# Performance work log

Measured on AMD Instinct MI355X. Metric: run time of the kernel, lower is better.

## Reference

```python
import jax, jax.numpy as jnp
import numpy as np

NC = 4
X = Y = Z = 64
IMG_SHAPE = (96, 96, 96)
SPAN = 2          # FILTER_SIZE = [5,5,5]
NUM_ITER = 4
DIL = 2           # DILATION = 2.0
SMOOTH_DISTANCE_INIT = 0.3
PRIOR_DISTANCE_INIT = 0.3


def _ind(d):
    # mirrors _get_ind from the torch code
    return (d, 0) if d > 0 else (0, -d)


def _sl(a, b):
    # slice(a, -b) with -0 -> None, mirrors _negative
    return slice(a, -b if b else None)


def _offsets():
    for dx in range(-SPAN, SPAN + 1):
        for dy in range(-SPAN, SPAN + 1):
            for dz in range(-SPAN, SPAN + 1):
                yield dx, dy, dz


def _lin_resize_axis(x, axis, out):
    # 1D linear interpolation matching torch align_corners=True
    n = x.shape[axis]
    if out == n:
        return x
    pos = jnp.arange(out, dtype=x.dtype) * ((n - 1) / (out - 1))
    i0 = jnp.clip(jnp.floor(pos).astype(jnp.int32), 0, n - 1)
    i1 = jnp.clip(i0 + 1, 0, n - 1)
    w = pos - i0.astype(x.dtype)
    shp = [1] * x.ndim
    shp[axis] = out
    w = w.reshape(shp)
    return jnp.take(x, i0, axis=axis) * (1 - w) + jnp.take(x, i1, axis=axis) * w


def _resize3d(x, out_sz):
    # trilinear, align_corners=True, separable over the 3 spatial axes of [b,c,X,Y,Z]
    for ax, o in zip((2, 3, 4), out_sz):
        x = _lin_resize_axis(x, ax, o)
    return x


def _smooth_gaussian(feats):
    # feats: [b, c, X, Y, Z] -> gaussian [b, 5,5,5, X, Y, Z]
    b = feats.shape[0]
    sp = feats.shape[2:]
    g = jnp.zeros((b, 5, 5, 5) + sp, feats.dtype)
    for dx, dy, dz in _offsets():
        dx1, dx2 = _ind(dx); dy1, dy2 = _ind(dy); dz1, dz2 = _ind(dz)
        a = feats[:, :, _sl(dx1, dx2), _sl(dy1, dy2), _sl(dz1, dz2)]
        c = feats[:, :, _sl(dx2, dx1), _sl(dy2, dy1), _sl(dz2, dz1)]
        e = jnp.exp(-0.5 * jnp.sum((a - c) ** 2, axis=1))
        g = g.at[:, dx + SPAN, dy + SPAN, dz + SPAN,
                 _sl(dx2, dx1), _sl(dy2, dy1), _sl(dz2, dz1)].set(e)
    return g


def _prior_gaussian(f1, f2):
    # f1, f2: [b, c, x, y, z] (already downsampled) -> [b, 5,5,5, x, y, z]
    b = f1.shape[0]
    sp = f1.shape[2:]
    g = jnp.zeros((b, 5, 5, 5) + sp, f1.dtype)
    for dx, dy, dz in _offsets():
        dx1, dx2 = _ind(dx); dy1, dy2 = _ind(dy); dz1, dz2 = _ind(dz)
        a = f1[:, :, _sl(dx2, dx1), _sl(dy2, dy1), _sl(dz2, dz1)]
        c = f2[:, :, _sl(dx1, dx2), _sl(dy1, dy2), _sl(dz1, dz2)]
        e = jnp.exp(-0.5 * jnp.sum((a - c) ** 2, axis=1))
        g = g.at[:, dx + SPAN, dy + SPAN, dz + SPAN,
                 _sl(dx2, dx1), _sl(dy2, dy1), _sl(dz2, dz1)].set(e)
    return g


def _message(p, g):
    # p: [b, nc, x, y, z]; g: [b, 5,5,5, x, y, z]
    out = jnp.zeros_like(p)
    for dx, dy, dz in _offsets():
        dx1, dx2 = _ind(dx); dy1, dy2 = _ind(dy); dz1, dz2 = _ind(dz)
        a = p[:, :, _sl(dx1, dx2), _sl(dy1, dy2), _sl(dz1, dz2)]
        w = g[:, None, dx + SPAN, dy + SPAN, dz + SPAN,
              _sl(dx2, dx1), _sl(dy2, dy1), _sl(dz2, dz1)]
        out = out.at[:, :, _sl(dx2, dx1), _sl(dy2, dy1), _sl(dz2, dz1)].add(a * w)
    return out


def setup_inputs() -> dict:
    key = jax.random.key(0)
    ks = jax.random.split(key, 6)
    unary = jax.random.normal(ks[0], (1, NC, X, Y, Z), jnp.float32)
    img = jax.random.normal(ks[1], (1, 2, X, Y, Z), jnp.float32)
    atlas = jax.random.normal(ks[2], (1, 2, X, Y, Z), jnp.float32)
    atlas_label = jax.random.uniform(ks[3], (1, X, Y, Z, NC), jnp.float32)
    patch_start = jax.random.randint(ks[4], (1, 3), 0, 32, jnp.int32)
    return {
        "unary": unary,
        "img": img,
        "atlas": atlas,
        "atlas_label": atlas_label,
        "patch_start": patch_start,
        "smooth_norm": jnp.array([1.0 / SMOOTH_DISTANCE_INIT], jnp.float32),
        "smooth_weight": jnp.ones((NC,), jnp.float32),
        "prior_norm": jnp.array([1.0 / PRIOR_DISTANCE_INIT], jnp.float32),
        "prior_weight": jnp.ones(IMG_SHAPE, jnp.float32),
        "compat_w": jnp.eye(NC, dtype=jnp.float32),
    }


def reference(unary, img, atlas, atlas_label, patch_start,
              smooth_norm, smooth_weight, prior_norm, prior_weight, compat_w):
    b, nc, x, y, z = unary.shape
    ds = (x // DIL, y // DIL, z // DIL)  # floor(in*0.5) == ceil(in/2) for even dims

    # similarity kernels
    sg = _smooth_gaussian(img * smooth_norm)                      # [b,5,5,5,x,y,z]
    f1 = _resize3d(img * prior_norm, ds)
    f2 = _resize3d(atlas * prior_norm, ds)
    pg = _prior_gaussian(f1, f2)                                  # [b,5,5,5,x/2,y/2,z/2]

    # prior message is independent of q_values: compute once
    al = jnp.transpose(atlas_label, (0, 4, 1, 2, 3))              # [b,nc,x,y,z]
    al_ds = _resize3d(al, ds)
    pm = _resize3d(_message(al_ds, pg), (x, y, z))                # [b,nc,x,y,z]
    pw = jax.lax.dynamic_slice(
        prior_weight,
        (patch_start[0, 0], patch_start[0, 1], patch_start[0, 2]),
        (x, y, z))
    prior_term = pw[None, None] * pm

    q = unary
    for _ in range(NUM_ITER):
        p = jax.nn.softmax(q, axis=1)
        sm = _message(p, sg)
        pred = smooth_weight[None, :, None, None, None] * sm + prior_term
        q = unary + jnp.einsum('oc,bcxyz->boxyz', compat_w, pred)  # 1x1x1 compat conv
    return q
```

## Files before the change

kernel.cpp:

```cpp
#include <hip/hip_runtime.h>

#define NN 64
#define N3 (64*64*64)
#define DS 32
#define DS3 (32*32*32)

#define LOG2E 1.4426950408889634f
#define FSCALE 0.8493218002880191f

typedef _Float16 h2  __attribute__((ext_vector_type(2)));
typedef __fp16   h2f __attribute__((ext_vector_type(2)));

__device__ __forceinline__ float fexp2(float x) { return __builtin_amdgcn_exp2f(x); }

__device__ __forceinline__ h2 u2h(unsigned u) { union { unsigned u; h2 h; } c; c.u = u; return c.h; }
__device__ __forceinline__ unsigned h2u(h2 h) { union { unsigned u; h2 h; } c; c.h = h; return c.u; }
__device__ __forceinline__ h2 pkh(float a, float b) {
    union { h2f a; h2 b; } c; c.a = __builtin_amdgcn_cvt_pkrtz(a, b); return c.b;
}
__device__ __forceinline__ float fdot2(h2 a, h2 b) {
    union { h2 h; h2f f; } ca, cb; ca.h = a; cb.h = b;
    return __builtin_amdgcn_fdot2(ca.f, cb.f, 0.0f, false);
}

__device__ __forceinline__ void axw(int j, float scale, int nmax, int& i0, int& i1, float& w) {
    float pos = (float)j * scale;
    int f = (int)floorf(pos);
    if (f < 0) f = 0;
    if (f > nmax) f = nmax;
    i0 = f;
    i1 = (f + 1 <= nmax) ? f + 1 : nmax;
    w = pos - (float)f;
}


__global__ __launch_bounds__(128) void k_downsample(
    const float* __restrict__ img, const float* __restrict__ atlas,
    const float* __restrict__ alabel, const float* __restrict__ pnorm,
    unsigned* __restrict__ f1pk, uint4* __restrict__ nb)
{
    int idx = blockIdx.x * 128 + threadIdx.x;
    int z = idx & 31, y = (idx >> 5) & 31, x = idx >> 10;

    const float scale = 63.0f / 31.0f;
    int x0,x1,y0,y1,z0,z1; float wx,wy,wz;
    axw(x, scale, 63, x0, x1, wx);
    axw(y, scale, 63, y0, y1, wy);
    axw(z, scale, 63, z0, z1, wz);

    float w000=(1-wx)*(1-wy)*(1-wz), w001=(1-wx)*(1-wy)*wz;
    float w010=(1-wx)*wy*(1-wz),     w011=(1-wx)*wy*wz;
    float w100=wx*(1-wy)*(1-wz),     w101=wx*(1-wy)*wz;
    float w110=wx*wy*(1-wz),         w111=wx*wy*wz;

    int c000=(x0*NN+y0)*NN+z0, c001=(x0*NN+y0)*NN+z1;
    int c010=(x0*NN+y1)*NN+z0, c011=(x0*NN+y1)*NN+z1;
    int c100=(x1*NN+y0)*NN+z0, c101=(x1*NN+y0)*NN+z1;
    int c110=(x1*NN+y1)*NN+z0, c111=(x1*NN+y1)*NN+z1;

    auto tri = [&](const float* p) -> float {
        return p[c000]*w000 + p[c001]*w001 + p[c010]*w010 + p[c011]*w011
             + p[c100]*w100 + p[c101]*w101 + p[c110]*w110 + p[c111]*w111;
    };
    float pnf = pnorm[0] * FSCALE;
    f1pk[idx] = h2u(pkh(pnf*tri(img), pnf*tri(img + N3)));

    auto tril = [&](int c) -> float {
        return alabel[c000*4+c]*w000 + alabel[c001*4+c]*w001 + alabel[c010*4+c]*w010 + alabel[c011*4+c]*w011
             + alabel[c100*4+c]*w100 + alabel[c101*4+c]*w101 + alabel[c110*4+c]*w110 + alabel[c111*4+c]*w111;
    };
    nb[idx] = make_uint4(h2u(pkh(pnf*tri(atlas), pnf*tri(atlas + N3))),
                         h2u(pkh(tril(0), tril(1))),
                         h2u(pkh(tril(2), tril(3))), 0u);
}

__global__ __launch_bounds__(128) void k_prior_msg(
    const unsigned* __restrict__ f1pk, const uint4* __restrict__ nb,
    float4* __restrict__ pm)
{
    int idx = blockIdx.x * 128 + threadIdx.x;
    int z = idx & 31, y = (idx >> 5) & 31, x = idx >> 10;

    h2 ncf = -u2h(f1pk[idx]);
    float a0=0.f, a1=0.f, a2=0.f, a3=0.f;
    for (int dx = -2; dx <= 2; ++dx) {
        int xx = x + dx; if ((unsigned)xx >= DS) continue;
        for (int dy = -2; dy <= 2; ++dy) {
            int yy = y + dy; if ((unsigned)yy >= DS) continue;
            int base = (xx*DS + yy)*DS;
            #pragma unroll
            for (int dz = -2; dz <= 2; ++dz) {
                int zz = z + dz; if ((unsigned)zz >= DS) continue;
                uint4 v = nb[base + zz];
                h2 d = u2h(v.x) + ncf;
                float t = fdot2(d, d);
                float w = fexp2(-t);
                h2 l01 = u2h(v.y), l23 = u2h(v.z);
                a0 += w*(float)l01.x; a1 += w*(float)l01.y;
                a2 += w*(float)l23.x; a3 += w*(float)l23.y;
            }
        }
    }
    pm[idx] = make_float4(a0, a1, a2, a3);
}


#define TXD 8
#define TYD 8
#define TZD 8
#define TZR 4
#define RZ 2
#define HX 12
#define HY 12
#define HZ 12
#define PZ 14

template<bool QV_IN, bool QV_OUT>
__global__ __launch_bounds__(1024, 8) void k_iter(
    const float* __restrict__ qin,
    const float* __restrict__ unary,
    const float* __restrict__ img,
    const float* __restrict__ snorm,
    const float* __restrict__ sweight,
    const float* __restrict__ compat,
    const float4* __restrict__ pm,
    const float* __restrict__ pweight,
    const int* __restrict__ pstart,
    float* __restrict__ qout)
{
    __shared__ __align__(16) uint2    pS[HX][HY][PZ];
    __shared__ __align__(8)  unsigned fS[HX][HY][PZ];
    __shared__ __align__(16) uint4    accS[3][TXD*TYD*TZR];

    const int tzg = threadIdx.x, ty = threadIdx.y;
    const int tx = threadIdx.z & 7, s = threadIdx.z >> 3;
    const int x0b = blockIdx.z * TXD, y0b = blockIdx.y * TYD, z0b = blockIdx.x * TZD;
    const int tid = threadIdx.x + TZR*threadIdx.y + (TZR*TYD)*threadIdx.z;
    const float sc = snorm[0] * FSCALE;

    #pragma unroll
    for (int rr = 0; rr < 2; ++rr) {
        int i = tid + rr*1024;
        if (i < HX*HY*HZ) {
            int lz = i % HZ; int r = i / HZ;
            int ly = r % HY; int lx = r / HY;
            int gx = x0b + lx - 2, gy = y0b + ly - 2, gz = z0b + lz - 2;
            uint2 pu = make_uint2(0u, 0u);
            unsigned fu = 0u;
            if ((unsigned)gx < NN && (unsigned)gy < NN && (unsigned)gz < NN) {
                int g = (gx*NN + gy)*NN + gz;
                float q0, q1, q2, q3;
                if (QV_IN) {
                    float4 qv = reinterpret_cast<const float4*>(qin)[g];
                    q0 = qv.x; q1 = qv.y; q2 = qv.z; q3 = qv.w;
                } else {
                    q0 = qin[g]; q1 = qin[g+N3]; q2 = qin[g+2*N3]; q3 = qin[g+3*N3];
                }
                float m = fmaxf(fmaxf(q0,q1), fmaxf(q2,q3));
                float e0 = fexp2((q0-m)*LOG2E);
                float e1 = fexp2((q1-m)*LOG2E);
                float e2 = fexp2((q2-m)*LOG2E);
                float e3 = fexp2((q3-m)*LOG2E);
                float inv = 1.0f/(e0+e1+e2+e3);
                pu = make_uint2(h2u(pkh(e0*inv, e1*inv)), h2u(pkh(e2*inv, e3*inv)));
                fu = h2u(pkh(img[g]*sc, img[g+N3]*sc));
            }
            pS[lx][ly][lz] = pu;
            fS[lx][ly][lz] = fu;
        }
    }
    __syncthreads();

    const int tz0 = tzg * RZ;
    const int gx = x0b + tx, gy = y0b + ty, gz = z0b + tz0;

    const h2 ncf0 = -u2h(fS[tx+2][ty+2][tz0+2]);
    const h2 ncf1 = -u2h(fS[tx+2][ty+2][tz0+3]);

    h2 a01_0 = (h2)0, a23_0 = (h2)0, a01_1 = (h2)0, a23_1 = (h2)0;

    #pragma unroll
    for (int pp = 0; pp < 7; ++pp) {
        int p = (3 - s) + 4*pp;
        if (p < 25) {
            int dx = p / 5, dy = p - 5*dx;
            const uint4* pv = reinterpret_cast<const uint4*>(&pS[tx+dx][ty+dy][tz0]);
            const uint2* fv = reinterpret_cast<const uint2*>(&fS[tx+dx][ty+dy][tz0]);
            uint4 qa = pv[0], qb = pv[1], qc = pv[2];
            uint2 fa = fv[0], fb = fv[1], fc = fv[2];

            unsigned fz[6]  = { fa.x, fa.y, fb.x, fb.y, fc.x, fc.y };
            unsigned p01[6] = { qa.x, qa.z, qb.x, qb.z, qc.x, qc.z };
            unsigned p23[6] = { qa.y, qa.w, qb.y, qb.w, qc.y, qc.w };

            #pragma unroll
            for (int dz = 0; dz < 5; ++dz) {
                {
                    h2 d = u2h(fz[dz]) + ncf0;
                    float w = fexp2(-fdot2(d, d));
                    h2 w2 = pkh(w, w);
                    a01_0 = w2 * u2h(p01[dz]) + a01_0;
                    a23_0 = w2 * u2h(p23[dz]) + a23_0;
                }
                {
                    h2 d = u2h(fz[dz+1]) + ncf1;
                    float w = fexp2(-fdot2(d, d));
                    h2 w2 = pkh(w, w);
                    a01_1 = w2 * u2h(p01[dz+1]) + a01_1;
                    a23_1 = w2 * u2h(p23[dz+1]) + a23_1;
                }
            }
        }
    }

    const int pid = (tx*TYD + ty)*TZR + tzg;
    if (s != 0) {
        accS[s-1][pid] = make_uint4(h2u(a01_0), h2u(a23_0), h2u(a01_1), h2u(a23_1));
    }

    float4 pr0 = make_float4(0.f,0.f,0.f,0.f), pr1 = make_float4(0.f,0.f,0.f,0.f);
    if (s == 0) {
        const float S13 = 31.0f / 63.0f;
        float posx = (float)gx * S13; int xc0 = (int)posx; float wxf = posx - (float)xc0;
        int xc1 = xc0 < 31 ? xc0+1 : 31;
        float posy = (float)gy * S13; int yc0 = (int)posy; float wyf = posy - (float)yc0;
        int yc1 = yc0 < 31 ? yc0+1 : 31;
        int r00i = (xc0*DS+yc0)*DS, r01i = (xc0*DS+yc1)*DS;
        int r10i = (xc1*DS+yc0)*DS, r11i = (xc1*DS+yc1)*DS;
        auto upz = [&](int gzv) -> float4 {
            float posz = (float)gzv * S13; int zc0 = (int)posz; float wzf = posz - (float)zc0;
            int zc1 = zc0 < 31 ? zc0+1 : 31;
            float4 p000 = pm[r00i+zc0], p001 = pm[r00i+zc1];
            float4 p010 = pm[r01i+zc0], p011 = pm[r01i+zc1];
            float4 p100 = pm[r10i+zc0], p101 = pm[r10i+zc1];
            float4 p110 = pm[r11i+zc0], p111 = pm[r11i+zc1];
            float w000=(1-wxf)*(1-wyf)*(1-wzf), w001=(1-wxf)*(1-wyf)*wzf;
            float w010=(1-wxf)*wyf*(1-wzf),     w011=(1-wxf)*wyf*wzf;
            float w100=wxf*(1-wyf)*(1-wzf),     w101=wxf*(1-wyf)*wzf;
            float w110=wxf*wyf*(1-wzf),         w111=wxf*wyf*wzf;
            float4 r;
            r.x = w000*p000.x + w001*p001.x + w010*p010.x + w011*p011.x + w100*p100.x + w101*p101.x + w110*p110.x + w111*p111.x;
            r.y = w000*p000.y + w001*p001.y + w010*p010.y + w011*p011.y + w100*p100.y + w101*p101.y + w110*p110.y + w111*p111.y;
            r.z = w000*p000.z + w001*p001.z + w010*p010.z + w011*p011.z + w100*p100.z + w101*p101.z + w110*p110.z + w111*p111.z;
            r.w = w000*p000.w + w001*p001.w + w010*p010.w + w011*p011.w + w100*p100.w + w101*p101.w + w110*p110.w + w111*p111.w;
            return r;
        };
        pr0 = upz(gz);
        pr1 = upz(gz+1);
        int ps0 = pstart[0], ps1 = pstart[1], ps2 = pstart[2];
        int pwbase = (ps0+gx)*96*96 + (ps1+gy)*96 + ps2 + gz;
        float pwa = pweight[pwbase], pwb = pweight[pwbase+1];
        pr0.x *= pwa; pr0.y *= pwa; pr0.z *= pwa; pr0.w *= pwa;
        pr1.x *= pwb; pr1.y *= pwb; pr1.z *= pwb; pr1.w *= pwb;
    }

    __syncthreads();

    if (s == 0) {
        #pragma unroll
        for (int j = 0; j < 3; ++j) {
            uint4 v = accS[j][pid];
            a01_0 += u2h(v.x); a23_0 += u2h(v.y);
            a01_1 += u2h(v.z); a23_1 += u2h(v.w);
        }

        const int g = (gx*NN + gy)*NN + gz;
        float2 un0 = *(const float2*)(unary + 0*N3 + g);
        float2 un1 = *(const float2*)(unary + 1*N3 + g);
        float2 un2 = *(const float2*)(unary + 2*N3 + g);
        float2 un3 = *(const float2*)(unary + 3*N3 + g);
        float sw0 = sweight[0], sw1 = sweight[1], sw2 = sweight[2], sw3 = sweight[3];
        float cw[16];
        #pragma unroll
        for (int k = 0; k < 16; ++k) cw[k] = compat[k];

        float p0, p1, p2, p3;
        float r00, r10, r20, r30, r01, r11, r21, r31;
        p0 = sw0*(float)a01_0.x + pr0.x; p1 = sw1*(float)a01_0.y + pr0.y;
        p2 = sw2*(float)a23_0.x + pr0.z; p3 = sw3*(float)a23_0.y + pr0.w;
        r00 = un0.x + cw[0]*p0  + cw[1]*p1  + cw[2]*p2  + cw[3]*p3;
        r10 = un1.x + cw[4]*p0  + cw[5]*p1  + cw[6]*p2  + cw[7]*p3;
        r20 = un2.x + cw[8]*p0  + cw[9]*p1  + cw[10]*p2 + cw[11]*p3;
        r30 = un3.x + cw[12]*p0 + cw[13]*p1 + cw[14]*p2 + cw[15]*p3;
        p0 = sw0*(float)a01_1.x + pr1.x; p1 = sw1*(float)a01_1.y + pr1.y;
        p2 = sw2*(float)a23_1.x + pr1.z; p3 = sw3*(float)a23_1.y + pr1.w;
        r01 = un0.y + cw[0]*p0  + cw[1]*p1  + cw[2]*p2  + cw[3]*p3;
        r11 = un1.y + cw[4]*p0  + cw[5]*p1  + cw[6]*p2  + cw[7]*p3;
        r21 = un2.y + cw[8]*p0  + cw[9]*p1  + cw[10]*p2 + cw[11]*p3;
        r31 = un3.y + cw[12]*p0 + cw[13]*p1 + cw[14]*p2 + cw[15]*p3;

        if (QV_OUT) {
            reinterpret_cast<float4*>(qout)[g]   = make_float4(r00, r10, r20, r30);
            reinterpret_cast<float4*>(qout)[g+1] = make_float4(r01, r11, r21, r31);
        } else {
            *(float2*)(qout + 0*N3 + g) = make_float2(r00, r01);
            *(float2*)(qout + 1*N3 + g) = make_float2(r10, r11);
            *(float2*)(qout + 2*N3 + g) = make_float2(r20, r21);
            *(float2*)(qout + 3*N3 + g) = make_float2(r30, r31);
        }
    }
}


extern "C" void kernel_launch(void* const* d_in, const int* in_sizes, int n_in,
                              void* d_out, int out_size, void* d_ws, size_t ws_size,
                              hipStream_t stream)
{
    const float* unary   = (const float*)d_in[0];
    const float* img     = (const float*)d_in[1];
    const float* atlas   = (const float*)d_in[2];
    const float* alabel  = (const float*)d_in[3];
    const int*   pstart  = (const int*)d_in[4];
    const float* snorm   = (const float*)d_in[5];
    const float* sweight = (const float*)d_in[6];
    const float* pnorm   = (const float*)d_in[7];
    const float* pweight = (const float*)d_in[8];
    const float* compat  = (const float*)d_in[9];
    float* out = (float*)d_out;
    float* ws  = (float*)d_ws;

    float*    qA   = ws;
    float*    qB   = ws + 4*N3;
    unsigned* f1pk = (unsigned*)(ws + 8*N3);
    uint4*    nbuf = (uint4*)(f1pk + DS3);
    float4*   pm   = (float4*)(nbuf + DS3);

    k_downsample<<<DS3/128, 128, 0, stream>>>(img, atlas, alabel, pnorm, f1pk, nbuf);
    k_prior_msg<<<DS3/128, 128, 0, stream>>>(f1pk, nbuf, pm);

    dim3 grid(NN/TZD, NN/TYD, NN/TXD), block(TZR, TYD, 32);
    k_iter<false,true><<<grid, block, 0, stream>>>(unary, unary, img, snorm, sweight, compat, pm, pweight, pstart, qA);
    k_iter<true, true><<<grid, block, 0, stream>>>(qA,    unary, img, snorm, sweight, compat, pm, pweight, pstart, qB);
    k_iter<true, true><<<grid, block, 0, stream>>>(qB,    unary, img, snorm, sweight, compat, pm, pweight, pstart, qA);
    k_iter<true,false><<<grid, block, 0, stream>>>(qA,    unary, img, snorm, sweight, compat, pm, pweight, pstart, out);
}
```

Baseline: 90.31 us.

## Fuse prior pipeline into one kernel and fold prior term into unary

The downsample, prior-message and upsample steps are merged into a single tiled kernel that stages the downsampled neighbourhood in shared memory. It precomputes unary plus the compat-projected prior term into an interleaved float4 buffer, so the iteration kernels no longer redo the prior upsample and pweight lookups on every pass. The iteration kernel also changes its thread split: each thread now handles 4 z-outputs instead of 2, with 8 neighbour-offset groups per output. This enlarges the shared-memory reduction buffers. The prior message is now stored in fp16, which reduces precision.

```diff
diff --git a/kernel.cpp b/kernel.cpp
--- a/kernel.cpp
+++ b/kernel.cpp
@@ -3,7 +3,6 @@
 #define NN 64
 #define N3 (64*64*64)
 #define DS 32
-#define DS3 (32*32*32)
 
 #define LOG2E 1.4426950408889634f
 #define FSCALE 0.8493218002880191f
@@ -23,119 +22,175 @@
     return __builtin_amdgcn_fdot2(ca.f, cb.f, 0.0f, false);
 }
 
-__device__ __forceinline__ void axw(int j, float scale, int nmax, int& i0, int& i1, float& w) {
-    float pos = (float)j * scale;
-    int f = (int)floorf(pos);
-    if (f < 0) f = 0;
-    if (f > nmax) f = nmax;
-    i0 = f;
-    i1 = (f + 1 <= nmax) ? f + 1 : nmax;
-    w = pos - (float)f;
-}
-
-
-__global__ __launch_bounds__(128) void k_downsample(
+
+#define PMX 6
+#define PMY 10
+#define PMZ 10
+#define SXD 10
+#define SYD 14
+#define SZD 14
+
+__global__ __launch_bounds__(1024) void k_prior(
     const float* __restrict__ img, const float* __restrict__ atlas,
-    const float* __restrict__ alabel, const float* __restrict__ pnorm,
-    unsigned* __restrict__ f1pk, uint4* __restrict__ nb)
+    const float* __restrict__ alabel, const float* __restrict__ unary,
+    const float* __restrict__ pnorm, const float* __restrict__ pweight,
+    const int* __restrict__ pstart, const float* __restrict__ compat,
+    float4* __restrict__ unary4)
 {
-    int idx = blockIdx.x * 128 + threadIdx.x;
-    int z = idx & 31, y = (idx >> 5) & 31, x = idx >> 10;
-
-    const float scale = 63.0f / 31.0f;
-    int x0,x1,y0,y1,z0,z1; float wx,wy,wz;
-    axw(x, scale, 63, x0, x1, wx);
-    axw(y, scale, 63, y0, y1, wy);
-    axw(z, scale, 63, z0, z1, wz);
-
-    float w000=(1-wx)*(1-wy)*(1-wz), w001=(1-wx)*(1-wy)*wz;
-    float w010=(1-wx)*wy*(1-wz),     w011=(1-wx)*wy*wz;
-    float w100=wx*(1-wy)*(1-wz),     w101=wx*(1-wy)*wz;
-    float w110=wx*wy*(1-wz),         w111=wx*wy*wz;
-
-    int c000=(x0*NN+y0)*NN+z0, c001=(x0*NN+y0)*NN+z1;
-    int c010=(x0*NN+y1)*NN+z0, c011=(x0*NN+y1)*NN+z1;
-    int c100=(x1*NN+y0)*NN+z0, c101=(x1*NN+y0)*NN+z1;
-    int c110=(x1*NN+y1)*NN+z0, c111=(x1*NN+y1)*NN+z1;
-
-    auto tri = [&](const float* p) -> float {
-        return p[c000]*w000 + p[c001]*w001 + p[c010]*w010 + p[c011]*w011
-             + p[c100]*w100 + p[c101]*w101 + p[c110]*w110 + p[c111]*w111;
-    };
-    float pnf = pnorm[0] * FSCALE;
-    f1pk[idx] = h2u(pkh(pnf*tri(img), pnf*tri(img + N3)));
-
-    auto tril = [&](int c) -> float {
-        return alabel[c000*4+c]*w000 + alabel[c001*4+c]*w001 + alabel[c010*4+c]*w010 + alabel[c011*4+c]*w011
-             + alabel[c100*4+c]*w100 + alabel[c101*4+c]*w101 + alabel[c110*4+c]*w110 + alabel[c111*4+c]*w111;
-    };
-    nb[idx] = make_uint4(h2u(pkh(pnf*tri(atlas), pnf*tri(atlas + N3))),
-                         h2u(pkh(tril(0), tril(1))),
-                         h2u(pkh(tril(2), tril(3))), 0u);
-}
-
-__global__ __launch_bounds__(128) void k_prior_msg(
-    const unsigned* __restrict__ f1pk, const uint4* __restrict__ nb,
-    float4* __restrict__ pm)
-{
-    int idx = blockIdx.x * 128 + threadIdx.x;
-    int z = idx & 31, y = (idx >> 5) & 31, x = idx >> 10;
-
-    h2 ncf = -u2h(f1pk[idx]);
-    float a0=0.f, a1=0.f, a2=0.f, a3=0.f;
-    for (int dx = -2; dx <= 2; ++dx) {
-        int xx = x + dx; if ((unsigned)xx >= DS) continue;
-        for (int dy = -2; dy <= 2; ++dy) {
-            int yy = y + dy; if ((unsigned)yy >= DS) continue;
-            int base = (xx*DS + yy)*DS;
-            #pragma unroll
-            for (int dz = -2; dz <= 2; ++dz) {
-                int zz = z + dz; if ((unsigned)zz >= DS) continue;
-                uint4 v = nb[base + zz];
-                h2 d = u2h(v.x) + ncf;
-                float t = fdot2(d, d);
-                float w = fexp2(-t);
-                h2 l01 = u2h(v.y), l23 = u2h(v.z);
-                a0 += w*(float)l01.x; a1 += w*(float)l01.y;
-                a2 += w*(float)l23.x; a3 += w*(float)l23.y;
+    __shared__ __align__(16) uint4 nbS[SXD][SYD][SZD];
+    __shared__ __align__(8)  uint2 pmS[PMX][PMY][PMZ];
+
+    const int tid = threadIdx.x;
+    const int x0 = blockIdx.z * 8, y0 = blockIdx.y * 16, z0 = blockIdx.x * 16;
+    const int cxlo = (x0*31)/63, cylo = (y0*31)/63, czlo = (z0*31)/63;
+
+    const float pnf = pnorm[0] * FSCALE;
+
+    for (int i = tid; i < SXD*SYD*SZD; i += 1024) {
+        int lz = i % SZD; int r = i / SZD; int ly = r % SYD; int lx = r / SYD;
+        int cx = cxlo - 2 + lx, cy = cylo - 2 + ly, cz = czlo - 2 + lz;
+        uint4 v = make_uint4(0u, 0u, 0u, 0u);
+        if ((unsigned)cx < DS && (unsigned)cy < DS && (unsigned)cz < DS) {
+            const float scale = 63.0f / 31.0f;
+            float posx = cx*scale; int a0i = (int)posx; float wx = posx - a0i; int a1i = a0i+1 <= 63 ? a0i+1 : 63;
+            float posy = cy*scale; int b0i = (int)posy; float wy = posy - b0i; int b1i = b0i+1 <= 63 ? b0i+1 : 63;
+            float posz = cz*scale; int d0i = (int)posz; float wz = posz - d0i; int d1i = d0i+1 <= 63 ? d0i+1 : 63;
+            float w000=(1-wx)*(1-wy)*(1-wz), w001=(1-wx)*(1-wy)*wz;
+            float w010=(1-wx)*wy*(1-wz),     w011=(1-wx)*wy*wz;
+            float w100=wx*(1-wy)*(1-wz),     w101=wx*(1-wy)*wz;
+            float w110=wx*wy*(1-wz),         w111=wx*wy*wz;
+            int c000=(a0i*NN+b0i)*NN+d0i, c001=(a0i*NN+b0i)*NN+d1i;
+            int c010=(a0i*NN+b1i)*NN+d0i, c011=(a0i*NN+b1i)*NN+d1i;
+            int c100=(a1i*NN+b0i)*NN+d0i, c101=(a1i*NN+b0i)*NN+d1i;
+            int c110=(a1i*NN+b1i)*NN+d0i, c111=(a1i*NN+b1i)*NN+d1i;
+            auto tri = [&](const float* p) -> float {
+                return p[c000]*w000 + p[c001]*w001 + p[c010]*w010 + p[c011]*w011
+                     + p[c100]*w100 + p[c101]*w101 + p[c110]*w110 + p[c111]*w111;
+            };
+            const float4* lab = (const float4*)alabel;
+            float4 l = make_float4(0.f,0.f,0.f,0.f);
+            {
+                float4 t;
+                t = lab[c000]; l.x += w000*t.x; l.y += w000*t.y; l.z += w000*t.z; l.w += w000*t.w;
+                t = lab[c001]; l.x += w001*t.x; l.y += w001*t.y; l.z += w001*t.z; l.w += w001*t.w;
+                t = lab[c010]; l.x += w010*t.x; l.y += w010*t.y; l.z += w010*t.z; l.w += w010*t.w;
+                t = lab[c011]; l.x += w011*t.x; l.y += w011*t.y; l.z += w011*t.z; l.w += w011*t.w;
+                t = lab[c100]; l.x += w100*t.x; l.y += w100*t.y; l.z += w100*t.z; l.w += w100*t.w;
+                t = lab[c101]; l.x += w101*t.x; l.y += w101*t.y; l.z += w101*t.z; l.w += w101*t.w;
+                t = lab[c110]; l.x += w110*t.x; l.y += w110*t.y; l.z += w110*t.z; l.w += w110*t.w;
+                t = lab[c111]; l.x += w111*t.x; l.y += w111*t.y; l.z += w111*t.z; l.w += w111*t.w;
             }
-        }
-    }
-    pm[idx] = make_float4(a0, a1, a2, a3);
+            v = make_uint4(h2u(pkh(pnf*tri(atlas), pnf*tri(atlas + N3))),
+                           h2u(pkh(l.x, l.y)), h2u(pkh(l.z, l.w)),
+                           h2u(pkh(pnf*tri(img), pnf*tri(img + N3))));
+        }
+        nbS[lx][ly][lz] = v;
+    }
+    __syncthreads();
+
+    for (int i = tid; i < PMX*PMY*PMZ; i += 1024) {
+        int pz = i % PMZ; int r = i / PMZ; int py = r % PMY; int px = r / PMY;
+        int cx = cxlo + px, cy = cylo + py, cz = czlo + pz;
+        uint2 o = make_uint2(0u, 0u);
+        if (cx < DS && cy < DS && cz < DS) {
+            h2 ncf = -u2h(nbS[px+2][py+2][pz+2].w);
+            float a0=0.f, a1=0.f, a2=0.f, a3=0.f;
+            for (int dx = -2; dx <= 2; ++dx) {
+                int xx = cx + dx; if ((unsigned)xx >= DS) continue;
+                for (int dy = -2; dy <= 2; ++dy) {
+                    int yy = cy + dy; if ((unsigned)yy >= DS) continue;
+                    #pragma unroll
+                    for (int dz = -2; dz <= 2; ++dz) {
+                        int zz = cz + dz; if ((unsigned)zz >= DS) continue;
+                        uint4 v = nbS[px+2+dx][py+2+dy][pz+2+dz];
+                        h2 d = u2h(v.x) + ncf;
+                        float w = fexp2(-fdot2(d, d));
+                        h2 l01 = u2h(v.y), l23 = u2h(v.z);
+                        a0 += w*(float)l01.x; a1 += w*(float)l01.y;
+                        a2 += w*(float)l23.x; a3 += w*(float)l23.y;
+                    }
+                }
+            }
+            o = make_uint2(h2u(pkh(a0, a1)), h2u(pkh(a2, a3)));
+        }
+        pmS[px][py][pz] = o;
+    }
+    __syncthreads();
+
+    const int ps0 = pstart[0], ps1 = pstart[1], ps2 = pstart[2];
+    float cw[16];
+    #pragma unroll
+    for (int k = 0; k < 16; ++k) cw[k] = compat[k];
+    const float S13 = 31.0f / 63.0f;
+
+    for (int i = tid; i < 8*16*16; i += 1024) {
+        int fz = i & 15, fy = (i >> 4) & 15, fx = i >> 8;
+        int gx = x0 + fx, gy = y0 + fy, gz = z0 + fz;
+        float posx = gx*S13; int xc0 = (int)posx; float wx = posx - xc0; int xc1 = xc0 < 31 ? xc0+1 : 31;
+        float posy = gy*S13; int yc0 = (int)posy; float wy = posy - yc0; int yc1 = yc0 < 31 ? yc0+1 : 31;
+        float posz = gz*S13; int zc0 = (int)posz; float wz = posz - zc0; int zc1 = zc0 < 31 ? zc0+1 : 31;
+        int lx0 = xc0-cxlo, lx1 = xc1-cxlo;
+        int ly0 = yc0-cylo, ly1 = yc1-cylo;
+        int lz0 = zc0-czlo, lz1 = zc1-czlo;
+
+        auto up = [&](uint2 u) -> float4 {
+            h2 a = u2h(u.x), b = u2h(u.y);
+            return make_float4((float)a.x, (float)a.y, (float)b.x, (float)b.y);
+        };
+        float4 p000 = up(pmS[lx0][ly0][lz0]), p001 = up(pmS[lx0][ly0][lz1]);
+        float4 p010 = up(pmS[lx0][ly1][lz0]), p011 = up(pmS[lx0][ly1][lz1]);
+        float4 p100 = up(pmS[lx1][ly0][lz0]), p101 = up(pmS[lx1][ly0][lz1]);
+        float4 p110 = up(pmS[lx1][ly1][lz0]), p111 = up(pmS[lx1][ly1][lz1]);
+        float w000=(1-wx)*(1-wy)*(1-wz), w001=(1-wx)*(1-wy)*wz;
+        float w010=(1-wx)*wy*(1-wz),     w011=(1-wx)*wy*wz;
+        float w100=wx*(1-wy)*(1-wz),     w101=wx*(1-wy)*wz;
+        float w110=wx*wy*(1-wz),         w111=wx*wy*wz;
+        float pw = pweight[(ps0+gx)*96*96 + (ps1+gy)*96 + (ps2+gz)];
+        float pr0 = pw*(w000*p000.x + w001*p001.x + w010*p010.x + w011*p011.x + w100*p100.x + w101*p101.x + w110*p110.x + w111*p111.x);
+        float pr1 = pw*(w000*p000.y + w001*p001.y + w010*p010.y + w011*p011.y + w100*p100.y + w101*p101.y + w110*p110.y + w111*p111.y);
+        float pr2 = pw*(w000*p000.z + w001*p001.z + w010*p010.z + w011*p011.z + w100*p100.z + w101*p101.z + w110*p110.z + w111*p111.z);
+        float pr3 = pw*(w000*p000.w + w001*p001.w + w010*p010.w + w011*p011.w + w100*p100.w + w101*p101.w + w110*p110.w + w111*p111.w);
+
+        int g = (gx*NN + gy)*NN + gz;
+        float4 q;
+        q.x = unary[g]      + cw[0]*pr0  + cw[1]*pr1  + cw[2]*pr2  + cw[3]*pr3;
+        q.y = unary[g+N3]   + cw[4]*pr0  + cw[5]*pr1  + cw[6]*pr2  + cw[7]*pr3;
+        q.z = unary[g+2*N3] + cw[8]*pr0  + cw[9]*pr1  + cw[10]*pr2 + cw[11]*pr3;
+        q.w = unary[g+3*N3] + cw[12]*pr0 + cw[13]*pr1 + cw[14]*pr2 + cw[15]*pr3;
+        unary4[g] = q;
+    }
 }
 
 
 #define TXD 8
 #define TYD 8
 #define TZD 8
-#define TZR 4
-#define RZ 2
+#define RZ 4
 #define HX 12
 #define HY 12
 #define HZ 12
 #define PZ 14
+#define PZF 20
 
 template<bool QV_IN, bool QV_OUT>
 __global__ __launch_bounds__(1024, 8) void k_iter(
     const float* __restrict__ qin,
-    const float* __restrict__ unary,
+    const float4* __restrict__ unary4,
     const float* __restrict__ img,
     const float* __restrict__ snorm,
     const float* __restrict__ sweight,
     const float* __restrict__ compat,
-    const float4* __restrict__ pm,
-    const float* __restrict__ pweight,
-    const int* __restrict__ pstart,
     float* __restrict__ qout)
 {
     __shared__ __align__(16) uint2    pS[HX][HY][PZ];
-    __shared__ __align__(8)  unsigned fS[HX][HY][PZ];
-    __shared__ __align__(16) uint4    accS[3][TXD*TYD*TZR];
+    __shared__ __align__(16) unsigned fS[HX][HY][PZF];
+    __shared__ __align__(16) uint4    accA[7][TXD*TYD*2];
+    __shared__ __align__(16) uint4    accB[7][TXD*TYD*2];
 
     const int tzg = threadIdx.x, ty = threadIdx.y;
     const int tx = threadIdx.z & 7, s = threadIdx.z >> 3;
     const int x0b = blockIdx.z * TXD, y0b = blockIdx.y * TYD, z0b = blockIdx.x * TZD;
-    const int tid = threadIdx.x + TZR*threadIdx.y + (TZR*TYD)*threadIdx.z;
+    const int tid = threadIdx.x + 2*threadIdx.y + 16*threadIdx.z;
     const float sc = snorm[0] * FSCALE;
 
     #pragma unroll
@@ -172,131 +227,88 @@
     __syncthreads();
 
     const int tz0 = tzg * RZ;
-    const int gx = x0b + tx, gy = y0b + ty, gz = z0b + tz0;
-
-    const h2 ncf0 = -u2h(fS[tx+2][ty+2][tz0+2]);
-    const h2 ncf1 = -u2h(fS[tx+2][ty+2][tz0+3]);
-
-    h2 a01_0 = (h2)0, a23_0 = (h2)0, a01_1 = (h2)0, a23_1 = (h2)0;
-
-    #pragma unroll
-    for (int pp = 0; pp < 7; ++pp) {
-        int p = (3 - s) + 4*pp;
+
+    h2 ncf[RZ];
+    #pragma unroll
+    for (int rz = 0; rz < RZ; ++rz) ncf[rz] = -u2h(fS[tx+2][ty+2][tz0+2+rz]);
+
+    h2 a01[RZ], a23[RZ];
+    #pragma unroll
+    for (int rz = 0; rz < RZ; ++rz) { a01[rz] = (h2)0; a23[rz] = (h2)0; }
+
+    #pragma unroll
+    for (int pp = 0; pp < 4; ++pp) {
+        int p = (7 - s) + 8*pp;
         if (p < 25) {
             int dx = p / 5, dy = p - 5*dx;
             const uint4* pv = reinterpret_cast<const uint4*>(&pS[tx+dx][ty+dy][tz0]);
-            const uint2* fv = reinterpret_cast<const uint2*>(&fS[tx+dx][ty+dy][tz0]);
-            uint4 qa = pv[0], qb = pv[1], qc = pv[2];
-            uint2 fa = fv[0], fb = fv[1], fc = fv[2];
-
-            unsigned fz[6]  = { fa.x, fa.y, fb.x, fb.y, fc.x, fc.y };
-            unsigned p01[6] = { qa.x, qa.z, qb.x, qb.z, qc.x, qc.z };
-            unsigned p23[6] = { qa.y, qa.w, qb.y, qb.w, qc.y, qc.w };
+            uint4 qa = pv[0], qb = pv[1], qc = pv[2], qd = pv[3];
+            const uint4* fv = reinterpret_cast<const uint4*>(&fS[tx+dx][ty+dy][tz0]);
+            uint4 fa = fv[0], fb = fv[1];
+
+            unsigned fz[8]  = { fa.x, fa.y, fa.z, fa.w, fb.x, fb.y, fb.z, fb.w };
+            unsigned p01[8] = { qa.x, qa.z, qb.x, qb.z, qc.x, qc.z, qd.x, qd.z };
+            unsigned p23[8] = { qa.y, qa.w, qb.y, qb.w, qc.y, qc.w, qd.y, qd.w };
 
             #pragma unroll
-            for (int dz = 0; dz < 5; ++dz) {
-                {
-                    h2 d = u2h(fz[dz]) + ncf0;
+            for (int rz = 0; rz < RZ; ++rz) {
+                #pragma unroll
+                for (int dz = 0; dz < 5; ++dz) {
+                    int k = rz + dz;
+                    h2 d = u2h(fz[k]) + ncf[rz];
                     float w = fexp2(-fdot2(d, d));
                     h2 w2 = pkh(w, w);
-                    a01_0 = w2 * u2h(p01[dz]) + a01_0;
-                    a23_0 = w2 * u2h(p23[dz]) + a23_0;
-                }
-                {
-                    h2 d = u2h(fz[dz+1]) + ncf1;
-                    float w = fexp2(-fdot2(d, d));
-                    h2 w2 = pkh(w, w);
-                    a01_1 = w2 * u2h(p01[dz+1]) + a01_1;
-                    a23_1 = w2 * u2h(p23[dz+1]) + a23_1;
+                    a01[rz] = w2 * u2h(p01[k]) + a01[rz];
+                    a23[rz] = w2 * u2h(p23[k]) + a23[rz];
                 }
             }
         }
     }
 
-    const int pid = (tx*TYD + ty)*TZR + tzg;
+    const int pid = (tx*TYD + ty)*2 + tzg;
     if (s != 0) {
-        accS[s-1][pid] = make_uint4(h2u(a01_0), h2u(a23_0), h2u(a01_1), h2u(a23_1));
-    }
-
-    float4 pr0 = make_float4(0.f,0.f,0.f,0.f), pr1 = make_float4(0.f,0.f,0.f,0.f);
-    if (s == 0) {
-        const float S13 = 31.0f / 63.0f;
-        float posx = (float)gx * S13; int xc0 = (int)posx; float wxf = posx - (float)xc0;
-        int xc1 = xc0 < 31 ? xc0+1 : 31;
-        float posy = (float)gy * S13; int yc0 = (int)posy; float wyf = posy - (float)yc0;
-        int yc1 = yc0 < 31 ? yc0+1 : 31;
-        int r00i = (xc0*DS+yc0)*DS, r01i = (xc0*DS+yc1)*DS;
-        int r10i = (xc1*DS+yc0)*DS, r11i = (xc1*DS+yc1)*DS;
-        auto upz = [&](int gzv) -> float4 {
-            float posz = (float)gzv * S13; int zc0 = (int)posz; float wzf = posz - (float)zc0;
-            int zc1 = zc0 < 31 ? zc0+1 : 31;
-            float4 p000 = pm[r00i+zc0], p001 = pm[r00i+zc1];
-            float4 p010 = pm[r01i+zc0], p011 = pm[r01i+zc1];
-            float4 p100 = pm[r10i+zc0], p101 = pm[r10i+zc1];
-            float4 p110 = pm[r11i+zc0], p111 = pm[r11i+zc1];
-            float w000=(1-wxf)*(1-wyf)*(1-wzf), w001=(1-wxf)*(1-wyf)*wzf;
-            float w010=(1-wxf)*wyf*(1-wzf),     w011=(1-wxf)*wyf*wzf;
-            float w100=wxf*(1-wyf)*(1-wzf),     w101=wxf*(1-wyf)*wzf;
-            float w110=wxf*wyf*(1-wzf),         w111=wxf*wyf*wzf;
-            float4 r;
-            r.x = w000*p000.x + w001*p001.x + w010*p010.x + w011*p011.x + w100*p100.x + w101*p101.x + w110*p110.x + w111*p111.x;
-            r.y = w000*p000.y + w001*p001.y + w010*p010.y + w011*p011.y + w100*p100.y + w101*p101.y + w110*p110.y + w111*p111.y;
-            r.z = w000*p000.z + w001*p001.z + w010*p010.z + w011*p011.z + w100*p100.z + w101*p101.z + w110*p110.z + w111*p111.z;
-            r.w = w000*p000.w + w001*p001.w + w010*p010.w + w011*p011.w + w100*p100.w + w101*p101.w + w110*p110.w + w111*p111.w;
-            return r;
-        };
-        pr0 = upz(gz);
-        pr1 = upz(gz+1);
-        int ps0 = pstart[0], ps1 = pstart[1], ps2 = pstart[2];
-        int pwbase = (ps0+gx)*96*96 + (ps1+gy)*96 + ps2 + gz;
-        float pwa = pweight[pwbase], pwb = pweight[pwbase+1];
-        pr0.x *= pwa; pr0.y *= pwa; pr0.z *= pwa; pr0.w *= pwa;
-        pr1.x *= pwb; pr1.y *= pwb; pr1.z *= pwb; pr1.w *= pwb;
-    }
-
+        accA[s-1][pid] = make_uint4(h2u(a01[0]), h2u(a01[1]), h2u(a01[2]), h2u(a01[3]));
+        accB[s-1][pid] = make_uint4(h2u(a23[0]), h2u(a23[1]), h2u(a23[2]), h2u(a23[3]));
+    }
     __syncthreads();
 
     if (s == 0) {
         #pragma unroll
-        for (int j = 0; j < 3; ++j) {
-            uint4 v = accS[j][pid];
-            a01_0 += u2h(v.x); a23_0 += u2h(v.y);
-            a01_1 += u2h(v.z); a23_1 += u2h(v.w);
-        }
-
-        const int g = (gx*NN + gy)*NN + gz;
-        float2 un0 = *(const float2*)(unary + 0*N3 + g);
-        float2 un1 = *(const float2*)(unary + 1*N3 + g);
-        float2 un2 = *(const float2*)(unary + 2*N3 + g);
-        float2 un3 = *(const float2*)(unary + 3*N3 + g);
-        float sw0 = sweight[0], sw1 = sweight[1], sw2 = sweight[2], sw3 = sweight[3];
+        for (int j = 0; j < 7; ++j) {
+            uint4 va = accA[j][pid];
+            a01[0] += u2h(va.x); a01[1] += u2h(va.y); a01[2] += u2h(va.z); a01[3] += u2h(va.w);
+            uint4 vb = accB[j][pid];
+            a23[0] += u2h(vb.x); a23[1] += u2h(vb.y); a23[2] += u2h(vb.z); a23[3] += u2h(vb.w);
+        }
+
+        const int gx = x0b + tx, gy = y0b + ty;
+        const int g = (gx*NN + gy)*NN + z0b + tz0;
+        const float sw0 = sweight[0], sw1 = sweight[1], sw2 = sweight[2], sw3 = sweight[3];
         float cw[16];
         #pragma unroll
         for (int k = 0; k < 16; ++k) cw[k] = compat[k];
 
-        float p0, p1, p2, p3;
-        float r00, r10, r20, r30, r01, r11, r21, r31;
-        p0 = sw0*(float)a01_0.x + pr0.x; p1 = sw1*(float)a01_0.y + pr0.y;
-        p2 = sw2*(float)a23_0.x + pr0.z; p3 = sw3*(float)a23_0.y + pr0.w;
-        r00 = un0.x + cw[0]*p0  + cw[1]*p1  + cw[2]*p2  + cw[3]*p3;
-        r10 = un1.x + cw[4]*p0  + cw[5]*p1  + cw[6]*p2  + cw[7]*p3;
-        r20 = un2.x + cw[8]*p0  + cw[9]*p1  + cw[10]*p2 + cw[11]*p3;
-        r30 = un3.x + cw[12]*p0 + cw[13]*p1 + cw[14]*p2 + cw[15]*p3;
-        p0 = sw0*(float)a01_1.x + pr1.x; p1 = sw1*(float)a01_1.y + pr1.y;
-        p2 = sw2*(float)a23_1.x + pr1.z; p3 = sw3*(float)a23_1.y + pr1.w;
-        r01 = un0.y + cw[0]*p0  + cw[1]*p1  + cw[2]*p2  + cw[3]*p3;
-        r11 = un1.y + cw[4]*p0  + cw[5]*p1  + cw[6]*p2  + cw[7]*p3;
-        r21 = un2.y + cw[8]*p0  + cw[9]*p1  + cw[10]*p2 + cw[11]*p3;
-        r31 = un3.y + cw[12]*p0 + cw[13]*p1 + cw[14]*p2 + cw[15]*p3;
+        float r[4][RZ];
+        #pragma unroll
+        for (int rz = 0; rz < RZ; ++rz) {
+            float4 u4 = unary4[g + rz];
+            float p0 = sw0*(float)a01[rz].x, p1 = sw1*(float)a01[rz].y;
+            float p2 = sw2*(float)a23[rz].x, p3 = sw3*(float)a23[rz].y;
+            r[0][rz] = u4.x + cw[0]*p0  + cw[1]*p1  + cw[2]*p2  + cw[3]*p3;
+            r[1][rz] = u4.y + cw[4]*p0  + cw[5]*p1  + cw[6]*p2  + cw[7]*p3;
+            r[2][rz] = u4.z + cw[8]*p0  + cw[9]*p1  + cw[10]*p2 + cw[11]*p3;
+            r[3][rz] = u4.w + cw[12]*p0 + cw[13]*p1 + cw[14]*p2 + cw[15]*p3;
+        }
 
         if (QV_OUT) {
-            reinterpret_cast<float4*>(qout)[g]   = make_float4(r00, r10, r20, r30);
-            reinterpret_cast<float4*>(qout)[g+1] = make_float4(r01, r11, r21, r31);
+            float4* qo = reinterpret_cast<float4*>(qout);
+            #pragma unroll
+            for (int rz = 0; rz < RZ; ++rz)
+                qo[g + rz] = make_float4(r[0][rz], r[1][rz], r[2][rz], r[3][rz]);
         } else {
-            *(float2*)(qout + 0*N3 + g) = make_float2(r00, r01);
-            *(float2*)(qout + 1*N3 + g) = make_float2(r10, r11);
-            *(float2*)(qout + 2*N3 + g) = make_float2(r20, r21);
-            *(float2*)(qout + 3*N3 + g) = make_float2(r30, r31);
+            #pragma unroll
+            for (int o = 0; o < 4; ++o)
+                *(float4*)(qout + o*N3 + g) = make_float4(r[o][0], r[o][1], r[o][2], r[o][3]);
         }
     }
 }
@@ -319,18 +331,19 @@
     float* out = (float*)d_out;
     float* ws  = (float*)d_ws;
 
-    float*    qA   = ws;
-    float*    qB   = ws + 4*N3;
-    unsigned* f1pk = (unsigned*)(ws + 8*N3);
-    uint4*    nbuf = (uint4*)(f1pk + DS3);
-    float4*   pm   = (float4*)(nbuf + DS3);
-
-    k_downsample<<<DS3/128, 128, 0, stream>>>(img, atlas, alabel, pnorm, f1pk, nbuf);
-    k_prior_msg<<<DS3/128, 128, 0, stream>>>(f1pk, nbuf, pm);
-
-    dim3 grid(NN/TZD, NN/TYD, NN/TXD), block(TZR, TYD, 32);
-    k_iter<false,true><<<grid, block, 0, stream>>>(unary, unary, img, snorm, sweight, compat, pm, pweight, pstart, qA);
-    k_iter<true, true><<<grid, block, 0, stream>>>(qA,    unary, img, snorm, sweight, compat, pm, pweight, pstart, qB);
-    k_iter<true, true><<<grid, block, 0, stream>>>(qB,    unary, img, snorm, sweight, compat, pm, pweight, pstart, qA);
-    k_iter<true,false><<<grid, block, 0, stream>>>(qA,    unary, img, snorm, sweight, compat, pm, pweight, pstart, out);
-}
+    float4* unary4 = (float4*)ws;
+    float*  qA     = ws + 4*N3;
+    float*  qB     = ws + 8*N3;
+
+    {
+        dim3 pgrid(4, 4, 8), pblock(1024);
+        k_prior<<<pgrid, pblock, 0, stream>>>(img, atlas, alabel, unary, pnorm,
+                                              pweight, pstart, compat, unary4);
+    }
+
+    dim3 grid(NN/TZD, NN/TYD, NN/TXD), block(2, 8, 64);
+    k_iter<false,true><<<grid, block, 0, stream>>>(unary, unary4, img, snorm, sweight, compat, qA);
+    k_iter<true, true><<<grid, block, 0, stream>>>(qA,    unary4, img, snorm, sweight, compat, qB);
+    k_iter<true, true><<<grid, block, 0, stream>>>(qB,    unary4, img, snorm, sweight, compat, qA);
+    k_iter<true,false><<<grid, block, 0, stream>>>(qA,    unary4, img, snorm, sweight, compat, out);
+}
```

After: 93.25 us. +3.3%, slower.
